# Performance work log

Measured on AMD Instinct MI355X. Metric: run time of the kernel, lower is better.

## Reference

```python
import jax, jax.numpy as jnp
import numpy as np
import math

E = 65536        # neighbor pairs (edges)
NAT = 2048       # atoms
NRAD = 24        # radial basis size
ZETA = [1, 2, 3, 4]
NCOMP = len(ZETA) + 1  # radial components: one 2-body + one per zeta
RCUT = 6.0
NELEM = 94       # one-hot element encoding size
EMB = 16         # species embedding dim


def _tables():
    """Static lxlylz enumeration per zeta: triples with lx+ly+lz = n, n in 0..z,
    multinomial/binomial normalization and (-1)^n lambda sign."""
    f = np.vectorize(math.factorial)
    tabs = []
    for z in ZETA:
        L = []
        for n in range(z + 1):
            for lx in range(n + 1):
                for ly in range(n - lx + 1):
                    L.append((lx, ly, n - lx - ly))
        L = np.array(L, np.int64)              # [K,3]
        nsum = L.sum(1)                        # [K]
        fact_lxlylz = f(L[:, 0]) * f(L[:, 1]) * f(L[:, 2])
        # (nfact/fact_lxlylz) * z!/((z-n)! n!) = z! / ((z-n)! * lx!ly!lz!)
        fact_norm = math.factorial(z) / (f(z - nsum) * fact_lxlylz)
        lam = (-1.0) ** nsum
        tabs.append((jnp.asarray(L, jnp.float32),
                     jnp.asarray(fact_norm, jnp.float32),
                     jnp.asarray(lam, jnp.float32)))
    return tabs

TABS = _tables()


def _forward(rij, Wr1, br1, Wr2, br2, Ws1, bs1, Ws2, bs2,
             Wa1, ba1, Wa2, ba2, Wa3, ba3, first_atom_idx, species_idx):
    nat = species_idx.shape[0]
    r = jnp.linalg.norm(rij, axis=1)                       # [E]
    u = rij / r[:, None]                                   # [E,3] unit vectors
    fc = 0.5 * (jnp.cos(jnp.pi * jnp.minimum(r, RCUT) / RCUT) + 1.0)
    centers = jnp.linspace(0.0, RCUT, NRAD, dtype=jnp.float32)
    width = RCUT / NRAD
    basis = jnp.exp(-((r[:, None] - centers) ** 2) / (2.0 * width * width)) * fc[:, None]  # [E,NRAD]
    # learned radial functions -> [E, NRAD, NCOMP]
    h = jax.nn.silu(basis @ Wr1 + br1)
    radial = jax.nn.silu(h @ Wr2 + br2).reshape(-1, NRAD, NCOMP)
    seg = first_atom_idx
    # two-body descriptor
    feats = [jax.ops.segment_sum(radial[:, :, 0], seg, num_segments=nat)]  # [nat,NRAD]
    for iz, z in enumerate(ZETA):
        L, fnorm, lam = TABS[iz]
        # g_ij over lxlylz combos: prod of powers of unit-vector components
        g_ij = jnp.prod((u[:, None, :] + 1e-12) ** L[None, :, :], axis=-1) * fnorm  # [E,K]
        g = jnp.einsum('er,ek->erk', radial[:, :, iz + 1], g_ij)                    # [E,NRAD,K]
        gi = jax.ops.segment_sum(g, seg, num_segments=nat)                          # [nat,NRAD,K]
        g2 = gi * gi
        norm = 2.0 ** (1.0 - z)
        feats.append(jnp.sum(g2, axis=-1) * norm)          # lambda = +1
        feats.append(jnp.sum(g2 * lam, axis=-1) * norm)    # lambda = -1
    feat = jnp.concatenate(feats, axis=1)                  # [nat, NRAD*(1+2*nzeta)]
    # species embedding and correlation
    onehot = jax.nn.one_hot(species_idx, NELEM, dtype=feat.dtype)
    emb = jax.nn.silu(onehot @ Ws1 + bs1) @ Ws2 + bs2      # [nat,EMB]
    x = (feat[:, :, None] * emb[:, None, :]).reshape(nat, -1)  # [nat, F*EMB]
    h = jax.nn.silu(x @ Wa1 + ba1)
    h = jax.nn.silu(h @ Wa2 + ba2)
    e = h @ Wa3 + ba3                                      # [nat,1] atomic energies
    return jnp.sum(e)                                      # total energy


def setup_inputs() -> dict:
    key = jax.random.key(0)
    ks = jax.random.split(key, 12)
    def w(k, shp):
        return jax.random.normal(k, shp, jnp.float32) / np.float32(np.sqrt(shp[0]))
    F = NRAD * (1 + 2 * len(ZETA)) * EMB  # 3456
    return {
        "rij": jax.random.normal(ks[0], (E, 3), jnp.float32) * 2.0,
        "Wr1": w(ks[1], (NRAD, 64)), "br1": jnp.zeros((64,), jnp.float32),
        "Wr2": w(ks[2], (64, NCOMP * NRAD)), "br2": jnp.zeros((NCOMP * NRAD,), jnp.float32),
        "Ws1": w(ks[3], (NELEM, 32)), "bs1": jnp.zeros((32,), jnp.float32),
        "Ws2": w(ks[4], (32, EMB)), "bs2": jnp.zeros((EMB,), jnp.float32),
        "Wa1": w(ks[5], (F, 256)), "ba1": jnp.zeros((256,), jnp.float32),
        "Wa2": w(ks[6], (256, 128)), "ba2": jnp.zeros((128,), jnp.float32),
        "Wa3": w(ks[7], (128, 1)), "ba3": jnp.zeros((1,), jnp.float32),
        "first_atom_idx": jnp.sort(jax.random.randint(ks[8], (E,), 0, NAT)),
        "species_idx": jax.random.randint(ks[9], (NAT,), 0, NELEM),
    }


def reference(rij, Wr1, br1, Wr2, br2, Ws1, bs1, Ws2, bs2,
              Wa1, ba1, Wa2, ba2, Wa3, ba3, first_atom_idx, species_idx):
    return _forward(rij, Wr1, br1, Wr2, br2, Ws1, bs1, Ws2, bs2,
                    Wa1, ba1, Wa2, ba2, Wa3, ba3, first_atom_idx, species_idx)
```

## Files before the change

### kernel.cpp

```cpp
#include <hip/hip_runtime.h>
#include <math.h>

#define KTOT 69
#define NRADC 24
#define NFEAT 216
#define NELEMC 94
#define EMBC 16
#define H1C 256
#define H2C 128
#define CE 16
#define EPR 20
#define KGN 18
#define GSTR 84
#define GISTR 76
#define TA 8
#define NPT 344

__device__ __constant__ int c_lx[KTOT] = {
  0,0,0,1,
  0,0,0,1,0,0,0,1,1,2,
  0,0,0,1,0,0,0,1,1,2,0,0,0,0,1,1,1,2,2,3,
  0,0,0,1,0,0,0,1,1,2,0,0,0,0,1,1,1,2,2,3,0,0,0,0,0,1,1,1,1,2,2,2,3,3,4};
__device__ __constant__ int c_ly[KTOT] = {
  0,0,1,0,
  0,0,1,0,0,1,2,0,1,0,
  0,0,1,0,0,1,2,0,1,0,0,1,2,3,0,1,2,0,1,0,
  0,0,1,0,0,1,2,0,1,0,0,1,2,3,0,1,2,0,1,0,0,1,2,3,4,0,1,2,3,0,1,2,0,1,0};
__device__ __constant__ int c_lz[KTOT] = {
  0,1,0,0,
  0,1,0,0,2,1,0,1,0,0,
  0,1,0,0,2,1,0,1,0,0,3,2,1,0,2,1,0,1,0,0,
  0,1,0,0,2,1,0,1,0,0,3,2,1,0,2,1,0,1,0,0,4,3,2,1,0,3,2,1,0,2,1,0,1,0,0};
__device__ __constant__ float c_fn[KTOT] = {
  1,1,1,1,
  1,2,2,2,1,2,1,2,2,1,
  1,3,3,3,3,6,3,6,6,3,1,3,3,1,3,6,3,3,3,1,
  1,4,4,4,6,12,6,12,12,6,4,12,12,4,12,24,12,12,12,4,
  1,4,6,4,1,4,12,12,4,6,12,6,4,4,1};
__device__ __constant__ float c_lam[KTOT] = {
  1,-1,-1,-1,
  1,-1,-1,-1,1,1,1,1,1,1,
  1,-1,-1,-1,1,1,1,1,1,1,-1,-1,-1,-1,-1,-1,-1,-1,-1,-1,
  1,-1,-1,-1,1,1,1,1,1,1,-1,-1,-1,-1,-1,-1,-1,-1,-1,-1,
  1,1,1,1,1,1,1,1,1,1,1,1,1,1,1};
__device__ __constant__ int c_k0[4] = {0,4,14,34};
__device__ __constant__ int c_kn[4] = {4,10,20,35};
__device__ __constant__ float c_zn[4] = {1.0f, 0.5f, 0.25f, 0.125f};
__device__ __constant__ int c_zidg[KGN] = {0, 1,1,1, 2,2,2,2,2, 3,3,3,3,3,3,3,3,3};

__device__ __forceinline__ float silu(float x) { return x / (1.0f + expf(-x)); }
__device__ __forceinline__ float4 silu4(float4 v) {
  v.x = silu(v.x); v.y = silu(v.y); v.z = silu(v.z); v.w = silu(v.w); return v;
}
__device__ __forceinline__ void fma4(float4& a, float s, const float4 w) {
  a.x += s * w.x; a.y += s * w.y; a.z += s * w.z; a.w += s * w.w;
}
__device__ __forceinline__ void fma44(float4& a, const float4 x, const float4 y) {
  a.x += x.x * y.x; a.y += x.y * y.y; a.z += x.z * y.z; a.w += x.w * y.w;
}
__device__ __forceinline__ float hsum4(const float4 v) { return (v.x + v.y) + (v.z + v.w); }
__device__ __forceinline__ float powsel(int l, float p, float p2, float p3, float p4) {
  float v = 1.0f;
  v = l >= 1 ? p : v;
  v = l >= 2 ? p2 : v;
  v = l >= 3 ? p3 : v;
  v = l >= 4 ? p4 : v;
  return v;
}

template <int NQ>
__device__ __forceinline__ void edge_l2(
    const float* __restrict__ s_h, const float* __restrict__ Wr2,
    const float* __restrict__ br2, float4* __restrict__ radial4,
    int e, int og, int eg, int E) {
  float4 acc[NQ];
  const float4* b2 = (const float4*)(br2 + og * 32);
  #pragma unroll
  for (int q = 0; q < NQ; ++q) acc[q] = b2[q];
  #pragma unroll 8
  for (int j = 0; j < 64; ++j) {
    float hv = s_h[e * 65 + j];
    const float4* w = (const float4*)(Wr2 + j * 120 + og * 32);
    #pragma unroll
    for (int q = 0; q < NQ; ++q) fma4(acc[q], hv, w[q]);
  }
  if (eg < E) {
    #pragma unroll
    for (int q = 0; q < NQ; ++q)
      radial4[(size_t)eg * 30 + og * 8 + q] = silu4(acc[q]);
  }
}

__global__ __launch_bounds__(256) void k_front(
    const float* __restrict__ rij,
    const float* __restrict__ Wr1, const float* __restrict__ br1,
    const float* __restrict__ Wr2, const float* __restrict__ br2,
    const int* __restrict__ fai, const int* __restrict__ spc,
    const float* __restrict__ Ws1, const float* __restrict__ bs1,
    const float* __restrict__ Ws2, const float* __restrict__ bs2,
    const float* __restrict__ Wa1,
    float4* __restrict__ radial4, int* __restrict__ bounds,
    int* __restrict__ porder, float* __restrict__ B,
    int E, int nat, int nbE, int nbB) {
  __shared__ __align__(16) float s_mem[64 * 25 + 64 * 65];
  const int blk = blockIdx.x;
  const int tid = threadIdx.x;

  if (blk < nbE) {
    float* s_bas = s_mem;
    float* s_h = s_mem + 64 * 25;
    const int e = tid & 63;
    const int og = __builtin_amdgcn_readfirstlane(tid >> 6);
    const int eg = blk * 64 + e;
    {
      float x = 0.0f, y = 0.0f, z = 0.0f;
      const bool ev = eg < E;
      if (ev) { x = rij[3 * eg]; y = rij[3 * eg + 1]; z = rij[3 * eg + 2]; }
      float r = sqrtf(x * x + y * y + z * z);
      float fcv = ev ? 0.5f * (cosf(3.14159265358979323846f * fminf(r, 6.0f) *
                                    (1.0f / 6.0f)) + 1.0f)
                     : 0.0f;
      #pragma unroll
      for (int t = 0; t < 6; ++t) {
        int m = og * 6 + t;
        float d = r - (6.0f / 23.0f) * (float)m;
        s_bas[e * 25 + m] = expf(-8.0f * d * d) * fcv;
      }
    }
    __syncthreads();
    {
      const float4* b1 = (const float4*)(br1 + og * 16);
      float4 acc[4] = {b1[0], b1[1], b1[2], b1[3]};
      #pragma unroll 8
      for (int m = 0; m < NRADC; ++m) {
        float b = s_bas[e * 25 + m];
        const float4* w = (const float4*)(Wr1 + m * 64 + og * 16);
        #pragma unroll
        for (int q = 0; q < 4; ++q) fma4(acc[q], b, w[q]);
      }
      #pragma unroll
      for (int q = 0; q < 4; ++q) {
        float4 v = silu4(acc[q]);
        float* dst = &s_h[e * 65 + og * 16 + 4 * q];
        dst[0] = v.x; dst[1] = v.y; dst[2] = v.z; dst[3] = v.w;
      }
    }
    __syncthreads();
    if (og < 3) edge_l2<8>(s_h, Wr2, br2, radial4, e, og, eg, E);
    else        edge_l2<6>(s_h, Wr2, br2, radial4, e, og, eg, E);
  } else if (blk < nbE + nbB) {
    int e = (blk - nbE) * 256 + tid;
    if (e < E) {
      int f = fai[e];
      int fp = (e == 0) ? -1 : fai[e - 1];
      for (int a = fp + 1; a <= f; ++a) bounds[a] = e;
      if (e == E - 1)
        for (int a = f + 1; a <= nat; ++a) bounds[a] = E;
    }
  } else if (blk == nbE + nbB) {
    int* s_cnt = (int*)s_mem;
    int* s_off = s_cnt + NELEMC;
    for (int i = tid; i < NELEMC; i += 256) s_cnt[i] = 0;
    __syncthreads();
    for (int a = tid; a < nat; a += 256) atomicAdd(&s_cnt[spc[a]], 1);
    __syncthreads();
    if (tid == 0) {
      int run = 0;
      for (int s = 0; s < NELEMC; ++s) {
        s_off[s] = run;
        run += ((s_cnt[s] + TA - 1) / TA) * TA;
      }
    }
    for (int i = tid; i < NPT * TA; i += 256) porder[i] = -1;
    __syncthreads();
    for (int a = tid; a < nat; a += 256) {
      int pos = atomicAdd(&s_off[spc[a]], 1);
      porder[pos] = a;
    }
  } else {
    float* s_hh = s_mem;
    float* s_emb = s_mem + 24 * 32;
    const int bi = blk - (nbE + nbB + 1);
    const int i = bi >> 2;
    const int sc0 = (bi & 3) * 24;
    const int scn = min(NELEMC, sc0 + 24) - sc0;
    const int o = tid;
    for (int idx = tid; idx < scn * 32; idx += 256) {
      int s = idx >> 5, c = idx & 31;
      s_hh[idx] = silu(Ws1[(sc0 + s) * 32 + c] + bs1[c]);
    }
    __syncthreads();
    for (int idx = tid; idx < scn * EMBC; idx += 256) {
      int s = idx >> 4, j = idx & 15;
      float acc = bs2[j];
      #pragma unroll
      for (int c = 0; c < 32; ++c) acc += s_hh[s * 32 + c] * Ws2[c * EMBC + j];
      s_emb[idx] = acc;
    }
    __syncthreads();
    float w[EMBC];
    #pragma unroll
    for (int j = 0; j < EMBC; ++j) w[j] = Wa1[(size_t)(i * EMBC + j) * H1C + o];
    for (int s = 0; s < scn; ++s) {
      float acc = 0.0f;
      #pragma unroll
      for (int j = 0; j < EMBC; ++j) acc += s_emb[s * EMBC + j] * w[j];
      B[((size_t)(sc0 + s) * NFEAT + i) * H1C + o] = acc;
    }
  }
}

__global__ __launch_bounds__(256) void k_atom(
    const float* __restrict__ rij,
    const float4* __restrict__ radial4,
    const int* __restrict__ bounds,
    float* __restrict__ feat, int E) {
  const int a = blockIdx.x;
  const int tid = threadIdx.x;
  __shared__ __align__(16) float s_radT[120 * EPR];
  __shared__ __align__(16) float s_gijT[KGN * GSTR];
  __shared__ __align__(16) float s_gi[NRADC * GISTR];
  __shared__ float s_feat[NFEAT];

  const int start = bounds[a];
  const int end = bounds[a + 1];

  const int e = tid & 15;
  const int sub = tid >> 4;

  const bool is_tile = tid < 216;
  const int eh = (tid < 216) ? (tid / 108) : 0;
  const int tile = (tid < 216) ? (tid % 108) : 0;
  const int rg = tile % 6;
  const int kg = tile / 6;
  const int comp0 = rg * 20 + 1 + c_zidg[kg];
  const bool is_2b = (tid >= 216 && tid < 240);
  const int rad2b = tid - 216;

  const int kstart = sub < 5 ? sub * 5 : 25 + (sub - 5) * 4;
  const int kcnt = sub < 5 ? 5 : 4;
  int t_pk[5], t_addr[5]; float t_fn[5];
  #pragma unroll
  for (int t = 0; t < 5; ++t) {
    int k = (t < kcnt) ? kstart + t : 0;
    t_pk[t] = c_lx[k] | (c_ly[k] << 8) | (c_lz[k] << 16);
    t_fn[t] = c_fn[k];
    int prow = k + (k < 14 ? 0 : 2);
    t_addr[t] = (prow >> 2) * GSTR + (prow & 3) * EPR + e;
  }

  const int pe0 = tid / 30, pc0 = tid - pe0 * 30;
  const int pe1 = (tid + 256) / 30, pc1 = (tid + 256) - pe1 * 30;

  if (tid < 60) {
    int rr = tid / EPR, ec = tid % EPR;
    int fkg = rr < 2 ? 3 : 17;
    int fj = rr < 2 ? 2 + rr : 3;
    s_gijT[fkg * GSTR + fj * EPR + ec] = 0.0f;
  }

  float4 acc[4][4];
  #pragma unroll
  for (int i = 0; i < 4; ++i)
    #pragma unroll
    for (int j = 0; j < 4; ++j) acc[i][j] = make_float4(0, 0, 0, 0);
  float4 acc2b = make_float4(0, 0, 0, 0);

  float4 pfA, pfB;
  float rx, ry, rz;
  auto prefetch = [&](int c0) {
    int lim = (end - c0) * 30;
    pfA = make_float4(0, 0, 0, 0);
    pfB = make_float4(0, 0, 0, 0);
    if (tid < lim) pfA = radial4[(size_t)c0 * 30 + tid];
    if (tid < 224 && tid + 256 < lim) pfB = radial4[(size_t)c0 * 30 + 256 + tid];
    int eg = c0 + e;
    rx = 0.0f; ry = 0.0f; rz = 0.0f;
    if (eg < end) { rx = rij[3 * eg]; ry = rij[3 * eg + 1]; rz = rij[3 * eg + 2]; }
  };
  prefetch(start);

  for (int c0 = start; c0 < end; c0 += CE) {
    __syncthreads();
    {
      int c = pc0 * 4;
      s_radT[(c + 0) * EPR + pe0] = pfA.x;
      s_radT[(c + 1) * EPR + pe0] = pfA.y;
      s_radT[(c + 2) * EPR + pe0] = pfA.z;
      s_radT[(c + 3) * EPR + pe0] = pfA.w;
      if (tid < 224) {
        int c2 = pc1 * 4;
        s_radT[(c2 + 0) * EPR + pe1] = pfB.x;
        s_radT[(c2 + 1) * EPR + pe1] = pfB.y;
        s_radT[(c2 + 2) * EPR + pe1] = pfB.z;
        s_radT[(c2 + 3) * EPR + pe1] = pfB.w;
      }
    }
    {
      const bool ev = (c0 + e) < end;
      float r = sqrtf(rx * rx + ry * ry + rz * rz);
      float inv = 1.0f / r;
      float px = rx * inv + 1e-12f, py = ry * inv + 1e-12f, pz = rz * inv + 1e-12f;
      float p2x = px * px, p3x = p2x * px, p4x = p2x * p2x;
      float p2y = py * py, p3y = p2y * py, p4y = p2y * p2y;
      float p2z = pz * pz, p3z = p2z * pz, p4z = p2z * p2z;
      #pragma unroll
      for (int t = 0; t < 5; ++t) {
        if (t < kcnt) {
          int pk = t_pk[t];
          float g = powsel(pk & 0xff, px, p2x, p3x, p4x) *
                    powsel((pk >> 8) & 0xff, py, p2y, p3y, p4y) *
                    powsel(pk >> 16, pz, p2z, p3z, p4z) * t_fn[t];
          s_gijT[t_addr[t]] = ev ? g : 0.0f;
        }
      }
    }
    __syncthreads();
    prefetch(c0 + CE);
    if (is_tile) {
      #pragma unroll
      for (int s = 0; s < 2; ++s) {
        int e0 = eh * 8 + s * 4;
        float4 gg[4];
        #pragma unroll
        for (int j = 0; j < 4; ++j)
          gg[j] = *(const float4*)&s_gijT[kg * GSTR + j * EPR + e0];
        #pragma unroll
        for (int i = 0; i < 4; ++i) {
          float4 rr = *(const float4*)&s_radT[(comp0 + 5 * i) * EPR + e0];
          #pragma unroll
          for (int j = 0; j < 4; ++j) fma44(acc[i][j], rr, gg[j]);
        }
      }
    }
    if (is_2b) {
      #pragma unroll
      for (int e0 = 0; e0 < 16; e0 += 4) {
        float4 v = *(const float4*)&s_radT[(rad2b * 5) * EPR + e0];
        acc2b.x += v.x; acc2b.y += v.y; acc2b.z += v.z; acc2b.w += v.w;
      }
    }
  }

  float4 hs[4];
  #pragma unroll
  for (int i = 0; i < 4; ++i)
    hs[i] = make_float4(hsum4(acc[i][0]), hsum4(acc[i][1]),
                        hsum4(acc[i][2]), hsum4(acc[i][3]));
  __syncthreads();
  if (is_tile && eh == 0) {
    #pragma unroll
    for (int i = 0; i < 4; ++i)
      *(float4*)&s_gi[(rg * 4 + i) * GISTR + kg * 4] = hs[i];
  }
  if (is_2b) s_feat[rad2b] = hsum4(acc2b);
  __syncthreads();
  if (is_tile && eh == 1) {
    #pragma unroll
    for (int i = 0; i < 4; ++i) {
      float4 v = *(const float4*)&s_gi[(rg * 4 + i) * GISTR + kg * 4];
      v.x += hs[i].x; v.y += hs[i].y; v.z += hs[i].z; v.w += hs[i].w;
      *(float4*)&s_gi[(rg * 4 + i) * GISTR + kg * 4] = v;
    }
  }
  __syncthreads();

  if (tid < 192) {
    int zb = tid / NRADC;
    int rad = tid - zb * NRADC;
    int z = zb >> 1;
    bool neg = zb & 1;
    int k0 = c_k0[z], kn = c_kn[z];
    float s = 0.0f;
    for (int k = k0; k < k0 + kn; ++k) {
      int prow = k + (k < 14 ? 0 : 2);
      float g = s_gi[rad * GISTR + prow];
      float g2 = g * g;
      s += neg ? g2 * c_lam[k] : g2;
    }
    s_feat[NRADC + zb * NRADC + rad] = s * c_zn[z];
  }
  __syncthreads();
  if (tid < NFEAT) feat[(size_t)a * NFEAT + tid] = s_feat[tid];
}

__global__ __launch_bounds__(256) void k_mlp(
    const float* __restrict__ feat, const float* __restrict__ B,
    const float* __restrict__ ba1, const float* __restrict__ Wa2,
    const float* __restrict__ ba2, const float* __restrict__ Wa3,
    const float* __restrict__ ba3, const int* __restrict__ porder,
    const int* __restrict__ sp, float* __restrict__ e_out) {
  const int nb = gridDim.x;
  int blk = blockIdx.x;
  if ((nb & 7) == 0) blk = (blockIdx.x & 7) * (nb >> 3) + (blockIdx.x >> 3);
  const int r0 = blk * TA;
  const int tid = threadIdx.x;
  __shared__ int s_a[TA];
  __shared__ __align__(16) float s_fT[NFEAT * TA];
  __shared__ __align__(16) float s_hT[H1C * TA];
  __shared__ float s_pre[TA][132];
  __shared__ float s_val[TA][132];
  if (tid < TA) s_a[tid] = porder[r0 + tid];
  __syncthreads();
  if (s_a[0] < 0) return;
  const int s = sp[s_a[0]];
  for (int idx = tid; idx < TA * 54; idx += 256) {
    int u = idx / 54, q = idx - u * 54;
    int a = s_a[u];
    float4 v = make_float4(0, 0, 0, 0);
    if (a >= 0) v = *(const float4*)(feat + (size_t)a * NFEAT + q * 4);
    s_fT[(q * 4 + 0) * TA + u] = v.x;
    s_fT[(q * 4 + 1) * TA + u] = v.y;
    s_fT[(q * 4 + 2) * TA + u] = v.z;
    s_fT[(q * 4 + 3) * TA + u] = v.w;
  }
  __syncthreads();
  {
    const int o = tid;
    float4 A0 = make_float4(0, 0, 0, 0), A1 = make_float4(0, 0, 0, 0);
    const float* Bp = B + ((size_t)s * NFEAT) * H1C + o;
    #pragma unroll 4
    for (int i = 0; i < NFEAT; ++i) {
      float bv = Bp[(size_t)i * H1C];
      float4 f0 = *(const float4*)&s_fT[i * TA];
      float4 f1 = *(const float4*)&s_fT[i * TA + 4];
      fma4(A0, bv, f0);
      fma4(A1, bv, f1);
    }
    const float b1v = ba1[o];
    *(float4*)&s_hT[o * TA] = silu4(make_float4(A0.x + b1v, A0.y + b1v,
                                                A0.z + b1v, A0.w + b1v));
    *(float4*)&s_hT[o * TA + 4] = silu4(make_float4(A1.x + b1v, A1.y + b1v,
                                                    A1.z + b1v, A1.w + b1v));
  }
  __syncthreads();
  {
    const int o = tid & 127;
    const int half = tid >> 7;
    float4 A0 = make_float4(0, 0, 0, 0), A1 = make_float4(0, 0, 0, 0);
    const int j0 = half * 128;
    #pragma unroll 4
    for (int j = j0; j < j0 + 128; ++j) {
      float wv = Wa2[j * H2C + o];
      float4 h0 = *(const float4*)&s_hT[j * TA];
      float4 hb = *(const float4*)&s_hT[j * TA + 4];
      fma4(A0, wv, h0);
      fma4(A1, wv, hb);
    }
    float pa[TA] = {A0.x, A0.y, A0.z, A0.w, A1.x, A1.y, A1.z, A1.w};
    if (half == 0) {
      #pragma unroll
      for (int u = 0; u < TA; ++u) s_pre[u][o] = pa[u];
    }
    __syncthreads();
    if (half == 1) {
      float b = ba2[o], w3 = Wa3[o];
      #pragma unroll
      for (int u = 0; u < TA; ++u)
        s_val[u][o] = silu(s_pre[u][o] + pa[u] + b) * w3;
    }
  }
  __syncthreads();
  if (tid < TA) {
    int a = s_a[tid];
    if (a >= 0) {
      float ss = 0.0f;
      for (int k = 0; k < H2C; ++k) ss += s_val[tid][k];
      e_out[a] = ss + ba3[0];
    }
  }
}

__global__ void k_reduce(const float* __restrict__ e_in, float* __restrict__ out, int nat) {
  int t = threadIdx.x;
  double acc = 0.0;
  for (int i = t; i < nat; i += 256) acc += (double)e_in[i];
  for (int o = 32; o; o >>= 1) acc += __shfl_down(acc, o, 64);
  __shared__ double s_par[4];
  if ((t & 63) == 0) s_par[t >> 6] = acc;
  __syncthreads();
  if (t == 0) out[0] = (float)(s_par[0] + s_par[1] + s_par[2] + s_par[3]);
}

extern "C" void kernel_launch(void* const* d_in, const int* in_sizes, int n_in,
                              void* d_out, int out_size, void* d_ws, size_t ws_size,
                              hipStream_t stream) {
  const float* rij = (const float*)d_in[0];
  const float* Wr1 = (const float*)d_in[1];
  const float* br1 = (const float*)d_in[2];
  const float* Wr2 = (const float*)d_in[3];
  const float* br2 = (const float*)d_in[4];
  const float* Ws1 = (const float*)d_in[5];
  const float* bs1 = (const float*)d_in[6];
  const float* Ws2 = (const float*)d_in[7];
  const float* bs2 = (const float*)d_in[8];
  const float* Wa1 = (const float*)d_in[9];
  const float* ba1 = (const float*)d_in[10];
  const float* Wa2 = (const float*)d_in[11];
  const float* ba2 = (const float*)d_in[12];
  const float* Wa3 = (const float*)d_in[13];
  const float* ba3 = (const float*)d_in[14];
  const int* fai = (const int*)d_in[15];
  const int* spc = (const int*)d_in[16];

  const int E = in_sizes[0] / 3;
  const int nat = in_sizes[16];

  float* ws = (float*)d_ws;
  size_t off = 0;
  float* radial = ws + off; off += (size_t)E * 120;
  float* feat = ws + off;  off += (size_t)nat * NFEAT;
  float* Bm = ws + off;    off += (size_t)NELEMC * NFEAT * H1C;
  float* e_ws = ws + off;  off += (size_t)nat;
  int* porder = (int*)(ws + off); off += (size_t)NPT * TA;
  int* bounds = (int*)(ws + off);

  const int nbE = (E + 63) / 64;
  const int nbB = (E + 255) / 256;
  k_front<<<nbE + nbB + 1 + NFEAT * 4, 256, 0, stream>>>(
      rij, Wr1, br1, Wr2, br2, fai, spc, Ws1, bs1, Ws2, bs2, Wa1,
      (float4*)radial, bounds, porder, Bm, E, nat, nbE, nbB);
  k_atom<<<nat, 256, 0, stream>>>(rij, (const float4*)radial, bounds, feat, E);
  k_mlp<<<NPT, 256, 0, stream>>>(feat, Bm, ba1, Wa2, ba2, Wa3, ba3,
                                 porder, spc, e_ws);
  k_reduce<<<1, 256, 0, stream>>>(e_ws, (float*)d_out, nat);
}
```

Before: 197.6 us.

## Fuse final energy reduction into MLP via atomics and read features directly

Drops the separate single-block reduction kernel. Each MLP block now sums its tile's atomic energies and atomically adds the total into the output, which is zeroed in the front kernel. The staging of the feature tile into shared memory is also removed, and features are read from global memory through wave-uniform per-atom pointers (scalar loads). This saves one launch and a shared-memory transpose, at the cost of float atomics that make the summation order nondeterministic and drop the double-precision accumulation.

Measured after the change: 202.6 us. 2.6% more time.

```diff
diff --git a/kernel.cpp b/kernel.cpp
--- a/kernel.cpp
+++ b/kernel.cpp
@@ -101,6 +101,7 @@
     const float* __restrict__ Wa1,
     float4* __restrict__ radial4, int* __restrict__ bounds,
     int* __restrict__ porder, float* __restrict__ B,
+    float* __restrict__ out0,
     int E, int nat, int nbE, int nbB) {
   __shared__ __align__(16) float s_mem[64 * 25 + 64 * 65];
   const int blk = blockIdx.x;
@@ -160,6 +161,7 @@
   } else if (blk == nbE + nbB) {
     int* s_cnt = (int*)s_mem;
     int* s_off = s_cnt + NELEMC;
+    if (tid == 0) out0[0] = 0.0f;
     for (int i = tid; i < NELEMC; i += 256) s_cnt[i] = 0;
     __syncthreads();
     for (int a = tid; a < nat; a += 256) atomicAdd(&s_cnt[spc[a]], 1);
@@ -389,32 +391,29 @@
     const float* __restrict__ ba1, const float* __restrict__ Wa2,
     const float* __restrict__ ba2, const float* __restrict__ Wa3,
     const float* __restrict__ ba3, const int* __restrict__ porder,
-    const int* __restrict__ sp, float* __restrict__ e_out) {
+    const int* __restrict__ sp, float* __restrict__ out0) {
   const int nb = gridDim.x;
   int blk = blockIdx.x;
   if ((nb & 7) == 0) blk = (blockIdx.x & 7) * (nb >> 3) + (blockIdx.x >> 3);
   const int r0 = blk * TA;
   const int tid = threadIdx.x;
   __shared__ int s_a[TA];
-  __shared__ __align__(16) float s_fT[NFEAT * TA];
   __shared__ __align__(16) float s_hT[H1C * TA];
   __shared__ float s_pre[TA][132];
   __shared__ float s_val[TA][132];
+  __shared__ float s_esum[TA];
   if (tid < TA) s_a[tid] = porder[r0 + tid];
   __syncthreads();
   if (s_a[0] < 0) return;
   const int s = sp[s_a[0]];
-  for (int idx = tid; idx < TA * 54; idx += 256) {
-    int u = idx / 54, q = idx - u * 54;
-    int a = s_a[u];
-    float4 v = make_float4(0, 0, 0, 0);
-    if (a >= 0) v = *(const float4*)(feat + (size_t)a * NFEAT + q * 4);
-    s_fT[(q * 4 + 0) * TA + u] = v.x;
-    s_fT[(q * 4 + 1) * TA + u] = v.y;
-    s_fT[(q * 4 + 2) * TA + u] = v.z;
-    s_fT[(q * 4 + 3) * TA + u] = v.w;
-  }
-  __syncthreads();
+  const float* fp[TA];
+  #pragma unroll
+  for (int u = 0; u < TA; ++u) {
+    int av = s_a[u];
+    av = (av < 0) ? s_a[0] : av;
+    av = __builtin_amdgcn_readfirstlane(av);
+    fp[u] = feat + (size_t)av * NFEAT;
+  }
   {
     const int o = tid;
     float4 A0 = make_float4(0, 0, 0, 0), A1 = make_float4(0, 0, 0, 0);
@@ -422,10 +421,10 @@
     #pragma unroll 4
     for (int i = 0; i < NFEAT; ++i) {
       float bv = Bp[(size_t)i * H1C];
-      float4 f0 = *(const float4*)&s_fT[i * TA];
-      float4 f1 = *(const float4*)&s_fT[i * TA + 4];
-      fma4(A0, bv, f0);
-      fma4(A1, bv, f1);
+      A0.x += fp[0][i] * bv;  A0.y += fp[1][i] * bv;
+      A0.z += fp[2][i] * bv;  A0.w += fp[3][i] * bv;
+      A1.x += fp[4][i] * bv;  A1.y += fp[5][i] * bv;
+      A1.z += fp[6][i] * bv;  A1.w += fp[7][i] * bv;
     }
     const float b1v = ba1[o];
     *(float4*)&s_hT[o * TA] = silu4(make_float4(A0.x + b1v, A0.y + b1v,
@@ -463,23 +462,20 @@
   __syncthreads();
   if (tid < TA) {
     int a = s_a[tid];
+    float ssum = 0.0f;
     if (a >= 0) {
-      float ss = 0.0f;
-      for (int k = 0; k < H2C; ++k) ss += s_val[tid][k];
-      e_out[a] = ss + ba3[0];
-    }
-  }
-}
-
-__global__ void k_reduce(const float* __restrict__ e_in, float* __restrict__ out, int nat) {
-  int t = threadIdx.x;
-  double acc = 0.0;
-  for (int i = t; i < nat; i += 256) acc += (double)e_in[i];
-  for (int o = 32; o; o >>= 1) acc += __shfl_down(acc, o, 64);
-  __shared__ double s_par[4];
-  if ((t & 63) == 0) s_par[t >> 6] = acc;
-  __syncthreads();
-  if (t == 0) out[0] = (float)(s_par[0] + s_par[1] + s_par[2] + s_par[3]);
+      for (int k = 0; k < H2C; ++k) ssum += s_val[tid][k];
+      ssum += ba3[0];
+    }
+    s_esum[tid] = ssum;
+  }
+  __syncthreads();
+  if (tid == 0) {
+    float tot = 0.0f;
+    #pragma unroll
+    for (int u = 0; u < TA; ++u) tot += s_esum[u];
+    atomicAdd(out0, tot);
+  }
 }
 
 extern "C" void kernel_launch(void* const* d_in, const int* in_sizes, int n_in,
@@ -511,7 +507,6 @@
   float* radial = ws + off; off += (size_t)E * 120;
   float* feat = ws + off;  off += (size_t)nat * NFEAT;
   float* Bm = ws + off;    off += (size_t)NELEMC * NFEAT * H1C;
-  float* e_ws = ws + off;  off += (size_t)nat;
   int* porder = (int*)(ws + off); off += (size_t)NPT * TA;
   int* bounds = (int*)(ws + off);
 
@@ -519,9 +514,8 @@
   const int nbB = (E + 255) / 256;
   k_front<<<nbE + nbB + 1 + NFEAT * 4, 256, 0, stream>>>(
       rij, Wr1, br1, Wr2, br2, fai, spc, Ws1, bs1, Ws2, bs2, Wa1,
-      (float4*)radial, bounds, porder, Bm, E, nat, nbE, nbB);
+      (float4*)radial, bounds, porder, Bm, (float*)d_out, E, nat, nbE, nbB);
   k_atom<<<nat, 256, 0, stream>>>(rij, (const float4*)radial, bounds, feat, E);
   k_mlp<<<NPT, 256, 0, stream>>>(feat, Bm, ba1, Wa2, ba2, Wa3, ba3,
-                                 porder, spc, e_ws);
-  k_reduce<<<1, 256, 0, stream>>>(e_ws, (float*)d_out, nat);
-}
+                                 porder, spc, (float*)d_out);
+}
```
